# Kernel optimization log

Measured on AMD Instinct MI355X. Metric: run time of the kernel, lower is better.

Reference implementation:

```python
import jax, jax.numpy as jnp
import numpy as np

N_NODES = 100000
N_EDGES = 1600000
IN_DIM = 64
OUT_DIM = 64


def setup_inputs() -> dict:
    key = jax.random.key(0)
    k1, k2, k3, k4, k5, k6 = jax.random.split(key, 6)
    x = jax.random.normal(k1, (N_NODES, IN_DIM), dtype=jnp.float32)
    edge_index = jax.random.randint(k2, (2, N_EDGES), 0, N_NODES, dtype=jnp.int64)
    s = 1.0 / np.sqrt(IN_DIM)
    W = jax.random.uniform(k3, (IN_DIM, OUT_DIM), minval=-s, maxval=s, dtype=jnp.float32)
    b = jax.random.uniform(k4, (OUT_DIM,), minval=-s, maxval=s, dtype=jnp.float32)
    W_lin = jax.random.uniform(k5, (IN_DIM, OUT_DIM), minval=-s, maxval=s, dtype=jnp.float32)
    b_lin = jax.random.uniform(k6, (OUT_DIM,), minval=-s, maxval=s, dtype=jnp.float32)
    return {"x": x, "edge_index": edge_index, "W": W, "b": b, "W_lin": W_lin, "b_lin": b_lin}


def _gcn_conv(x, edge_index, W, b):
    # GCNConv with self-loops and symmetric normalization:
    # out = D^{-1/2} (A + I) D^{-1/2} (x @ W) + b
    n = x.shape[0]
    loop = jnp.arange(n, dtype=edge_index.dtype)
    src = jnp.concatenate([edge_index[0], loop])  # [E+N]
    dst = jnp.concatenate([edge_index[1], loop])  # [E+N]
    deg = jax.ops.segment_sum(jnp.ones_like(src, dtype=x.dtype), dst, num_segments=n)
    dinv = jax.lax.rsqrt(jnp.maximum(deg, 1.0))  # deg >= 1 due to self-loops
    norm = dinv[src] * dinv[dst]                  # [E+N]
    h = x @ W                                     # [N, out]
    msg = h[src] * norm[:, None]                  # gather + scale
    out = jax.ops.segment_sum(msg, dst, num_segments=n)  # scatter-add
    return out + b


def reference(x, edge_index, W, b, W_lin, b_lin):
    # NaOp.forward with with_linear=True: conv(x, edge_index) + linear(x)
    return _gcn_conv(x, edge_index, W, b) + (x @ W_lin + b_lin)
```

## Files before the change

kernel.cpp:

```cpp
#include <hip/hip_runtime.h>

#define NN 100000
#define NE 1600000
#define DIM 64
#define K 782
#define ABLK 6250
#define NTILE 256
#define GCAP 2600

typedef __attribute__((ext_vector_type(8))) short bf16x8;
typedef __attribute__((ext_vector_type(2))) float f32x2;
typedef __attribute__((ext_vector_type(4))) float f32x4;

__device__ __forceinline__ unsigned short f2bf(float f) {
    union { float f; unsigned u; } c; c.f = f;
    unsigned r = (c.u + 0x7FFFu + ((c.u >> 16) & 1u)) >> 16;
    return (unsigned short)r;
}
__device__ __forceinline__ unsigned char f2fp8(float f) {
    int v = __builtin_amdgcn_cvt_pk_fp8_f32(f, f, 0, false);
    return (unsigned char)(v & 0xFF);
}
__device__ __forceinline__ void acc8(uint2 v, float& a0, float& a1, float& a2, float& a3,
                                     float& a4, float& a5, float& a6, float& a7) {
    f32x2 d0 = __builtin_amdgcn_cvt_pk_f32_fp8(v.x, false);
    f32x2 d1 = __builtin_amdgcn_cvt_pk_f32_fp8(v.x, true);
    f32x2 d2 = __builtin_amdgcn_cvt_pk_f32_fp8(v.y, false);
    f32x2 d3 = __builtin_amdgcn_cvt_pk_f32_fp8(v.y, true);
    a0 += d0.x; a1 += d0.y; a2 += d1.x; a3 += d1.y;
    a4 += d2.x; a5 += d2.y; a6 += d3.x; a7 += d3.y;
}


__global__ __launch_bounds__(1024) void k_binA(const int* __restrict__ ei,
                                               int* __restrict__ gcur,
                                               unsigned* __restrict__ ebuf) {
    __shared__ int hist[1024];
    __shared__ int hoff[K];
    __shared__ int gbase[K];
    __shared__ int lcur[K];
    __shared__ unsigned sbufE[ABLK];
    __shared__ unsigned short sbufB[ABLK];

    const int tid = threadIdx.x;
    const int e0 = blockIdx.x * ABLK;

    hist[tid] = 0;
    __syncthreads();

    int pk_[7]; int b_[7]; int myN = 0;
#pragma unroll
    for (int i = 0; i < 7; ++i) {
        int j = i * 1024 + tid;
        if (j < ABLK) {
            int e = e0 + j;
            int dst = ei[NE + e];
            int src = ei[e];
            int b = dst >> 7;
            pk_[myN]  = ((dst & 127) << 17) | src;
            b_[myN]   = b;
            ++myN;
            atomicAdd(&hist[b], 1);
        }
    }
    __syncthreads();

    int cntv = hist[tid];
    __syncthreads();
    for (int off = 1; off < 1024; off <<= 1) {
        int a = (tid >= off) ? hist[tid - off] : 0;
        __syncthreads();
        hist[tid] += a;
        __syncthreads();
    }
    if (tid < K) {
        int ho = hist[tid] - cntv;
        hoff[tid] = ho;
        lcur[tid] = ho;
        int claimed = (cntv > 0) ? atomicAdd(&gcur[tid], cntv) : 0;
        gbase[tid] = tid * GCAP + claimed;
    }
    __syncthreads();

    for (int j = 0; j < myN; ++j) {
        int pos = atomicAdd(&lcur[b_[j]], 1);
        sbufE[pos] = (unsigned)pk_[j];
        sbufB[pos] = (unsigned short)b_[j];
    }
    __syncthreads();

    for (int j = tid; j < ABLK; j += 1024) {
        unsigned en = sbufE[j];
        int b = sbufB[j];
        ebuf[gbase[b] + (j - hoff[b])] = en;
    }
}


__global__ __launch_bounds__(512) void k_gemm(
    const float* __restrict__ x, const float* __restrict__ W,
    const float* __restrict__ b, const float* __restrict__ Wl,
    const float* __restrict__ bl, const int* __restrict__ gcur,
    const unsigned* __restrict__ ebuf, int* __restrict__ ldeg,
    unsigned char* __restrict__ g8, float* __restrict__ out) {
    __shared__ unsigned short WcT[128][72];
    __shared__ int lcnt[128];

    const int tid = threadIdx.x;
    {
        const float4* W4  = (const float4*)W;
        const float4* Wl4 = (const float4*)Wl;
        for (int i = tid; i < 1024; i += 512) {
            int k  = i >> 4;
            int c0 = (i & 15) << 2;
            float4 wv = W4[i];
            float4 lv = Wl4[i];
            WcT[c0 + 0][k] = f2bf(wv.x); WcT[c0 + 1][k] = f2bf(wv.y);
            WcT[c0 + 2][k] = f2bf(wv.z); WcT[c0 + 3][k] = f2bf(wv.w);
            WcT[64 + c0 + 0][k] = f2bf(lv.x); WcT[64 + c0 + 1][k] = f2bf(lv.y);
            WcT[64 + c0 + 2][k] = f2bf(lv.z); WcT[64 + c0 + 3][k] = f2bf(lv.w);
        }
    }
    if (tid < 128) lcnt[tid] = 0;
    __syncthreads();

    const int base = blockIdx.x * GCAP;
    const int mB = gcur[blockIdx.x];
    for (int i = tid; i < mB; i += 512) {
        atomicAdd(&lcnt[ebuf[base + i] >> 17], 1);
    }

    const int wv_  = tid >> 6;
    const int lane = tid & 63;
    const int lr   = lane & 15;
    const int lkb  = (lane >> 4) << 3;

    const int lo   = blockIdx.x << 7;
    const int row0 = lo + wv_ * 16;

    int arow = row0 + lr;
    int arc  = arow < NN ? arow : NN - 1;
    const float* xp = x + (size_t)arc * DIM + lkb;
    float4 p0 = *(const float4*)(xp);
    float4 p1 = *(const float4*)(xp + 4);
    float4 p2 = *(const float4*)(xp + 32);
    float4 p3 = *(const float4*)(xp + 36);
    bf16x8 a0 = {(short)f2bf(p0.x), (short)f2bf(p0.y), (short)f2bf(p0.z), (short)f2bf(p0.w),
                 (short)f2bf(p1.x), (short)f2bf(p1.y), (short)f2bf(p1.z), (short)f2bf(p1.w)};
    bf16x8 a1 = {(short)f2bf(p2.x), (short)f2bf(p2.y), (short)f2bf(p2.z), (short)f2bf(p2.w),
                 (short)f2bf(p3.x), (short)f2bf(p3.y), (short)f2bf(p3.z), (short)f2bf(p3.w)};

    f32x4 acc[8];
#pragma unroll
    for (int ct = 0; ct < 8; ++ct) acc[ct] = (f32x4){0.f, 0.f, 0.f, 0.f};

#pragma unroll
    for (int ct = 0; ct < 8; ++ct) {
        bf16x8 b0 = *(const bf16x8*)&WcT[ct * 16 + lr][lkb];
        bf16x8 b1 = *(const bf16x8*)&WcT[ct * 16 + lr][32 + lkb];
        acc[ct] = __builtin_amdgcn_mfma_f32_16x16x32_bf16(a0, b0, acc[ct], 0, 0, 0);
        acc[ct] = __builtin_amdgcn_mfma_f32_16x16x32_bf16(a1, b1, acc[ct], 0, 0, 0);
    }
    __syncthreads();

    if (wv_ == 0) {
        int c0 = lcnt[lane];
        int c1 = lcnt[64 + lane];
        int v0 = c0;
        for (int off = 1; off < 64; off <<= 1) {
            int t = __shfl_up(v0, off);
            if (lane >= off) v0 += t;
        }
        int tot0 = __shfl(v0, 63);
        int v1 = c1;
        for (int off = 1; off < 64; off <<= 1) {
            int t = __shfl_up(v1, off);
            if (lane >= off) v1 += t;
        }
        int* lp = ldeg + blockIdx.x * 128;
        lp[lane] = v0 - c0;
        lp[64 + lane] = tot0 + v1 - c1;
    }

    float bcv[4];
#pragma unroll
    for (int ct = 0; ct < 4; ++ct) {
        int oc = ct * 16 + lr;
        bcv[ct] = b[oc] + bl[oc];
    }
    const int rbase = row0 + ((lane >> 4) << 2);
#pragma unroll
    for (int i = 0; i < 4; ++i) {
        int r = rbase + i;
        if (r >= NN) continue;
        float dv = rsqrtf((float)(lcnt[r - lo] + 1));
#pragma unroll
        for (int ct = 0; ct < 4; ++ct) {
            int oc = ct * 16 + lr;
            float accW = acc[ct][i];
            float accL = acc[ct + 4][i];
            float gvv = accW * dv;
            g8[(size_t)r * DIM + oc] = f2fp8(gvv);
            out[(size_t)r * DIM + oc] = accL + bcv[ct] + dv * gvv;
        }
    }
}


__global__ __launch_bounds__(512) void k_gatherB(
    const int* __restrict__ gcur, const unsigned* __restrict__ ebuf,
    const int* __restrict__ ldeg,
    const unsigned char* __restrict__ g8, float* __restrict__ out) {
    __shared__ int lptr[128];
    __shared__ int lcur[128];
    __shared__ unsigned lsrc[GCAP];

    const int tid = threadIdx.x;
    const int lo = blockIdx.x << 7;
    const int base = blockIdx.x * GCAP;
    const int mB = gcur[blockIdx.x];

    if (tid < 128) {
        int v = ldeg[blockIdx.x * 128 + tid];
        lptr[tid] = v;
        lcur[tid] = v;
    }
    __syncthreads();

    for (int i = tid; i < mB; i += 512) {
        unsigned en = ebuf[base + i];
        int ld = en >> 17;
        int pos = atomicAdd(&lcur[ld], 1);
        lsrc[pos] = en & 0x1FFFFu;
    }
    __syncthreads();

    const int w   = tid >> 6;
    const int lane = tid & 63;
    const int grp = lane >> 3;
    const int sub = lane & 7;
    const int sh  = sub << 3;

    const int nodeA = (w << 3) + grp;
    const int nodeB = 64 + nodeA;
    const int startA = lptr[nodeA];
    const int mA = lcur[nodeA] - startA;
    const int startB = lptr[nodeB];
    const int mBn = lcur[nodeB] - startB;

    float aA0 = 0.f, aA1 = 0.f, aA2 = 0.f, aA3 = 0.f, aA4 = 0.f, aA5 = 0.f, aA6 = 0.f, aA7 = 0.f;
    float aB0 = 0.f, aB1 = 0.f, aB2 = 0.f, aB3 = 0.f, aB4 = 0.f, aB5 = 0.f, aB6 = 0.f, aB7 = 0.f;

    int tA = 0, tB = 0;
    while (tA + 4 <= mA && tB + 4 <= mBn) {
        int sa0 = lsrc[startA + tA + 0], sa1 = lsrc[startA + tA + 1];
        int sa2 = lsrc[startA + tA + 2], sa3 = lsrc[startA + tA + 3];
        int sb0 = lsrc[startB + tB + 0], sb1 = lsrc[startB + tB + 1];
        int sb2 = lsrc[startB + tB + 2], sb3 = lsrc[startB + tB + 3];
        uint2 vA0 = *(const uint2*)(g8 + (((size_t)sa0) << 6) + sh);
        uint2 vA1 = *(const uint2*)(g8 + (((size_t)sa1) << 6) + sh);
        uint2 vA2 = *(const uint2*)(g8 + (((size_t)sa2) << 6) + sh);
        uint2 vA3 = *(const uint2*)(g8 + (((size_t)sa3) << 6) + sh);
        uint2 vB0 = *(const uint2*)(g8 + (((size_t)sb0) << 6) + sh);
        uint2 vB1 = *(const uint2*)(g8 + (((size_t)sb1) << 6) + sh);
        uint2 vB2 = *(const uint2*)(g8 + (((size_t)sb2) << 6) + sh);
        uint2 vB3 = *(const uint2*)(g8 + (((size_t)sb3) << 6) + sh);
        acc8(vA0, aA0, aA1, aA2, aA3, aA4, aA5, aA6, aA7);
        acc8(vA1, aA0, aA1, aA2, aA3, aA4, aA5, aA6, aA7);
        acc8(vA2, aA0, aA1, aA2, aA3, aA4, aA5, aA6, aA7);
        acc8(vA3, aA0, aA1, aA2, aA3, aA4, aA5, aA6, aA7);
        acc8(vB0, aB0, aB1, aB2, aB3, aB4, aB5, aB6, aB7);
        acc8(vB1, aB0, aB1, aB2, aB3, aB4, aB5, aB6, aB7);
        acc8(vB2, aB0, aB1, aB2, aB3, aB4, aB5, aB6, aB7);
        acc8(vB3, aB0, aB1, aB2, aB3, aB4, aB5, aB6, aB7);
        tA += 4; tB += 4;
    }
    while (tA + 4 <= mA) {
        int s0 = lsrc[startA + tA + 0], s1 = lsrc[startA + tA + 1];
        int s2 = lsrc[startA + tA + 2], s3 = lsrc[startA + tA + 3];
        uint2 v0 = *(const uint2*)(g8 + (((size_t)s0) << 6) + sh);
        uint2 v1 = *(const uint2*)(g8 + (((size_t)s1) << 6) + sh);
        uint2 v2 = *(const uint2*)(g8 + (((size_t)s2) << 6) + sh);
        uint2 v3 = *(const uint2*)(g8 + (((size_t)s3) << 6) + sh);
        acc8(v0, aA0, aA1, aA2, aA3, aA4, aA5, aA6, aA7);
        acc8(v1, aA0, aA1, aA2, aA3, aA4, aA5, aA6, aA7);
        acc8(v2, aA0, aA1, aA2, aA3, aA4, aA5, aA6, aA7);
        acc8(v3, aA0, aA1, aA2, aA3, aA4, aA5, aA6, aA7);
        tA += 4;
    }
    while (tB + 4 <= mBn) {
        int s0 = lsrc[startB + tB + 0], s1 = lsrc[startB + tB + 1];
        int s2 = lsrc[startB + tB + 2], s3 = lsrc[startB + tB + 3];
        uint2 v0 = *(const uint2*)(g8 + (((size_t)s0) << 6) + sh);
        uint2 v1 = *(const uint2*)(g8 + (((size_t)s1) << 6) + sh);
        uint2 v2 = *(const uint2*)(g8 + (((size_t)s2) << 6) + sh);
        uint2 v3 = *(const uint2*)(g8 + (((size_t)s3) << 6) + sh);
        acc8(v0, aB0, aB1, aB2, aB3, aB4, aB5, aB6, aB7);
        acc8(v1, aB0, aB1, aB2, aB3, aB4, aB5, aB6, aB7);
        acc8(v2, aB0, aB1, aB2, aB3, aB4, aB5, aB6, aB7);
        acc8(v3, aB0, aB1, aB2, aB3, aB4, aB5, aB6, aB7);
        tB += 4;
    }
    for (; tA < mA; ++tA) {
        uint2 v = *(const uint2*)(g8 + (((size_t)lsrc[startA + tA]) << 6) + sh);
        acc8(v, aA0, aA1, aA2, aA3, aA4, aA5, aA6, aA7);
    }
    for (; tB < mBn; ++tB) {
        uint2 v = *(const uint2*)(g8 + (((size_t)lsrc[startB + tB]) << 6) + sh);
        acc8(v, aB0, aB1, aB2, aB3, aB4, aB5, aB6, aB7);
    }

    {
        int gnode = lo + nodeA;
        if (gnode < NN) {
            float dv = rsqrtf((float)(mA + 1));
            float* op = out + (size_t)gnode * DIM + sh;
            float4 o0 = *(float4*)op;
            float4 o1 = *(float4*)(op + 4);
            o0.x += dv * aA0; o0.y += dv * aA1; o0.z += dv * aA2; o0.w += dv * aA3;
            o1.x += dv * aA4; o1.y += dv * aA5; o1.z += dv * aA6; o1.w += dv * aA7;
            *(float4*)op = o0;
            *(float4*)(op + 4) = o1;
        }
    }
    {
        int gnode = lo + nodeB;
        if (gnode < NN) {
            float dv = rsqrtf((float)(mBn + 1));
            float* op = out + (size_t)gnode * DIM + sh;
            float4 o0 = *(float4*)op;
            float4 o1 = *(float4*)(op + 4);
            o0.x += dv * aB0; o0.y += dv * aB1; o0.z += dv * aB2; o0.w += dv * aB3;
            o1.x += dv * aB4; o1.y += dv * aB5; o1.z += dv * aB6; o1.w += dv * aB7;
            *(float4*)op = o0;
            *(float4*)(op + 4) = o1;
        }
    }
}


extern "C" void kernel_launch(void* const* d_in, const int* in_sizes, int n_in,
                              void* d_out, int out_size, void* d_ws, size_t ws_size,
                              hipStream_t stream) {
    const float* x  = (const float*)d_in[0];
    const int*   ei = (const int*)d_in[1];
    const float* W  = (const float*)d_in[2];
    const float* b  = (const float*)d_in[3];
    const float* Wl = (const float*)d_in[4];
    const float* bl = (const float*)d_in[5];
    float* out = (float*)d_out;

    char* ws = (char*)d_ws;
    int*      gcur = (int*)(ws + 0);
    int*      ldeg = (int*)(ws + 4096);
    unsigned* ebuf = (unsigned*)(ws + 1048576);
    unsigned char* g8 = (unsigned char*)(ws + 10485760);

    hipMemsetAsync(gcur, 0, K * sizeof(int), stream);
    k_binA   <<<NTILE, 1024, 0, stream>>>(ei, gcur, ebuf);
    k_gemm   <<<K, 512, 0, stream>>>(x, W, b, Wl, bl, gcur, ebuf, ldeg, g8, out);
    k_gatherB<<<K, 512, 0, stream>>>(gcur, ebuf, ldeg, g8, out);
}
```

Measured before the change: 71.33 us.

## Stage linear term in fp16 buffer, pack fp8 stores, shuffle-based scan, kernel init

The GEMM kernel now writes the linear-plus-bias-plus-self-loop term as fp16 into a workspace buffer instead of fp32 into the output. The gather kernel reads that fp16 buffer and writes the final output once, so the output no longer needs a read-modify-write. FP8 g values are packed four per 32-bit store, and the block histogram scan uses wave shuffles instead of a barrier-heavy loop. The hipMemsetAsync is replaced by a small init kernel. Storing the intermediate in fp16 adds rounding error, and the gather's output stores are reorganised into strided float2 writes.

```diff
diff --git a/kernel.cpp b/kernel.cpp
--- a/kernel.cpp
+++ b/kernel.cpp
@@ -9,6 +9,7 @@
 #define GCAP 2600
 
 typedef __attribute__((ext_vector_type(8))) short bf16x8;
+typedef __attribute__((ext_vector_type(8))) _Float16 f16x8;
 typedef __attribute__((ext_vector_type(2))) float f32x2;
 typedef __attribute__((ext_vector_type(4))) float f32x4;
 
@@ -17,9 +18,9 @@
     unsigned r = (c.u + 0x7FFFu + ((c.u >> 16) & 1u)) >> 16;
     return (unsigned short)r;
 }
-__device__ __forceinline__ unsigned char f2fp8(float f) {
-    int v = __builtin_amdgcn_cvt_pk_fp8_f32(f, f, 0, false);
-    return (unsigned char)(v & 0xFF);
+__device__ __forceinline__ unsigned short f2h(float f) {
+    union { _Float16 h; unsigned short u; } c; c.h = (_Float16)f;
+    return c.u;
 }
 __device__ __forceinline__ void acc8(uint2 v, float& a0, float& a1, float& a2, float& a3,
                                      float& a4, float& a5, float& a6, float& a7) {
@@ -32,10 +33,17 @@
 }
 
 
+__global__ void k_init(int* __restrict__ gcur) {
+    int i = blockIdx.x * blockDim.x + threadIdx.x;
+    if (i < K) gcur[i] = 0;
+}
+
+
 __global__ __launch_bounds__(1024) void k_binA(const int* __restrict__ ei,
                                                int* __restrict__ gcur,
                                                unsigned* __restrict__ ebuf) {
     __shared__ int hist[1024];
+    __shared__ int wsum[16];
     __shared__ int hoff[K];
     __shared__ int gbase[K];
     __shared__ int lcur[K];
@@ -65,16 +73,25 @@
     }
     __syncthreads();
 
+    const int lane = tid & 63;
+    const int wid  = tid >> 6;
     int cntv = hist[tid];
-    __syncthreads();
-    for (int off = 1; off < 1024; off <<= 1) {
-        int a = (tid >= off) ? hist[tid - off] : 0;
-        __syncthreads();
-        hist[tid] += a;
-        __syncthreads();
+    int v = cntv;
+#pragma unroll
+    for (int off = 1; off < 64; off <<= 1) {
+        int t = __shfl_up(v, off);
+        if (lane >= off) v += t;
+    }
+    if (lane == 63) wsum[wid] = v;
+    __syncthreads();
+    int woff = 0;
+#pragma unroll
+    for (int u = 0; u < 15; ++u) {
+        if (u < wid) woff += wsum[u];
     }
     if (tid < K) {
-        int ho = hist[tid] - cntv;
+        int incl = v + woff;
+        int ho = incl - cntv;
         hoff[tid] = ho;
         lcur[tid] = ho;
         int claimed = (cntv > 0) ? atomicAdd(&gcur[tid], cntv) : 0;
@@ -102,7 +119,7 @@
     const float* __restrict__ b, const float* __restrict__ Wl,
     const float* __restrict__ bl, const int* __restrict__ gcur,
     const unsigned* __restrict__ ebuf, int* __restrict__ ldeg,
-    unsigned char* __restrict__ g8, float* __restrict__ out) {
+    unsigned char* __restrict__ g8, unsigned short* __restrict__ linbuf) {
     __shared__ unsigned short WcT[128][72];
     __shared__ int lcnt[128];
 
@@ -194,22 +211,24 @@
         int r = rbase + i;
         if (r >= NN) continue;
         float dv = rsqrtf((float)(lcnt[r - lo] + 1));
-#pragma unroll
-        for (int ct = 0; ct < 4; ++ct) {
-            int oc = ct * 16 + lr;
-            float accW = acc[ct][i];
-            float accL = acc[ct + 4][i];
-            float gvv = accW * dv;
-            g8[(size_t)r * DIM + oc] = f2fp8(gvv);
-            out[(size_t)r * DIM + oc] = accL + bcv[ct] + dv * gvv;
-        }
+        float gv0 = acc[0][i] * dv, gv1 = acc[1][i] * dv;
+        float gv2 = acc[2][i] * dv, gv3 = acc[3][i] * dv;
+        unsigned w32 = __builtin_amdgcn_cvt_pk_fp8_f32(gv0, gv1, 0, false);
+        w32 = (unsigned)__builtin_amdgcn_cvt_pk_fp8_f32(gv2, gv3, w32, true);
+        *(unsigned*)(g8 + ((size_t)r << 6) + (lr << 2)) = w32;
+        ushort4 lh;
+        lh.x = f2h(acc[4][i] + bcv[0] + dv * gv0);
+        lh.y = f2h(acc[5][i] + bcv[1] + dv * gv1);
+        lh.z = f2h(acc[6][i] + bcv[2] + dv * gv2);
+        lh.w = f2h(acc[7][i] + bcv[3] + dv * gv3);
+        *(ushort4*)(linbuf + ((size_t)r << 6) + (lr << 2)) = lh;
     }
 }
 
 
 __global__ __launch_bounds__(512) void k_gatherB(
     const int* __restrict__ gcur, const unsigned* __restrict__ ebuf,
-    const int* __restrict__ ldeg,
+    const int* __restrict__ ldeg, const unsigned short* __restrict__ linbuf,
     const unsigned char* __restrict__ g8, float* __restrict__ out) {
     __shared__ int lptr[128];
     __shared__ int lcur[128];
@@ -314,26 +333,32 @@
         int gnode = lo + nodeA;
         if (gnode < NN) {
             float dv = rsqrtf((float)(mA + 1));
-            float* op = out + (size_t)gnode * DIM + sh;
-            float4 o0 = *(float4*)op;
-            float4 o1 = *(float4*)(op + 4);
-            o0.x += dv * aA0; o0.y += dv * aA1; o0.z += dv * aA2; o0.w += dv * aA3;
-            o1.x += dv * aA4; o1.y += dv * aA5; o1.z += dv * aA6; o1.w += dv * aA7;
-            *(float4*)op = o0;
-            *(float4*)(op + 4) = o1;
+            f16x8 lf = *(const f16x8*)(linbuf + ((size_t)gnode << 6) + sh);
+            float* op = out + ((size_t)gnode << 6) + (sub << 1);
+            float2 o0 = {(float)lf[0] + dv * aA0, (float)lf[4] + dv * aA4};
+            float2 o1 = {(float)lf[1] + dv * aA1, (float)lf[5] + dv * aA5};
+            float2 o2 = {(float)lf[2] + dv * aA2, (float)lf[6] + dv * aA6};
+            float2 o3 = {(float)lf[3] + dv * aA3, (float)lf[7] + dv * aA7};
+            *(float2*)(op + 0)  = o0;
+            *(float2*)(op + 16) = o1;
+            *(float2*)(op + 32) = o2;
+            *(float2*)(op + 48) = o3;
         }
     }
     {
         int gnode = lo + nodeB;
         if (gnode < NN) {
             float dv = rsqrtf((float)(mBn + 1));
-            float* op = out + (size_t)gnode * DIM + sh;
-            float4 o0 = *(float4*)op;
-            float4 o1 = *(float4*)(op + 4);
-            o0.x += dv * aB0; o0.y += dv * aB1; o0.z += dv * aB2; o0.w += dv * aB3;
-            o1.x += dv * aB4; o1.y += dv * aB5; o1.z += dv * aB6; o1.w += dv * aB7;
-            *(float4*)op = o0;
-            *(float4*)(op + 4) = o1;
+            f16x8 lf = *(const f16x8*)(linbuf + ((size_t)gnode << 6) + sh);
+            float* op = out + ((size_t)gnode << 6) + (sub << 1);
+            float2 o0 = {(float)lf[0] + dv * aB0, (float)lf[4] + dv * aB4};
+            float2 o1 = {(float)lf[1] + dv * aB1, (float)lf[5] + dv * aB5};
+            float2 o2 = {(float)lf[2] + dv * aB2, (float)lf[6] + dv * aB6};
+            float2 o3 = {(float)lf[3] + dv * aB3, (float)lf[7] + dv * aB7};
+            *(float2*)(op + 0)  = o0;
+            *(float2*)(op + 16) = o1;
+            *(float2*)(op + 32) = o2;
+            *(float2*)(op + 48) = o3;
         }
     }
 }
@@ -354,10 +379,11 @@
     int*      gcur = (int*)(ws + 0);
     int*      ldeg = (int*)(ws + 4096);
     unsigned* ebuf = (unsigned*)(ws + 1048576);
-    unsigned char* g8 = (unsigned char*)(ws + 10485760);
-
-    hipMemsetAsync(gcur, 0, K * sizeof(int), stream);
+    unsigned char*  g8     = (unsigned char*)(ws + 10485760);
+    unsigned short* linbuf = (unsigned short*)(ws + 17039360);
+
+    k_init   <<<1, 1024, 0, stream>>>(gcur);
     k_binA   <<<NTILE, 1024, 0, stream>>>(ei, gcur, ebuf);
-    k_gemm   <<<K, 512, 0, stream>>>(x, W, b, Wl, bl, gcur, ebuf, ldeg, g8, out);
-    k_gatherB<<<K, 512, 0, stream>>>(gcur, ebuf, ldeg, g8, out);
-}
+    k_gemm   <<<K, 512, 0, stream>>>(x, W, b, Wl, bl, gcur, ebuf, ldeg, g8, linbuf);
+    k_gatherB<<<K, 512, 0, stream>>>(gcur, ebuf, ldeg, linbuf, g8, out);
+}
```

Result: faster. 69.03 us (-3.2%).
